# Optimization experiments

Hardware: AMD Instinct MI355X
Metric: run time of the kernel (lower is better)

Reference implementation:

```python
import jax, jax.numpy as jnp
import numpy as np

B, T, DIM, H, BUCKET = 4, 4096, 1024, 16, 64
E = DIM // H          # head dim = 64
U = T // BUCKET       # number of buckets = 64
EPS = 1e-6


def setup_inputs() -> dict:
    key = jax.random.key(0)
    ks = jax.random.split(key, 5)
    scale = 1.0 / np.sqrt(DIM)
    return {
        "x": jax.random.normal(ks[0], (B, T, DIM), dtype=jnp.float32),
        "Wq": jax.random.normal(ks[1], (DIM, DIM), dtype=jnp.float32) * scale,
        "Wk": jax.random.normal(ks[2], (DIM, DIM), dtype=jnp.float32) * scale,
        "Wv": jax.random.normal(ks[3], (DIM, DIM), dtype=jnp.float32) * scale,
        "Wo": jax.random.normal(ks[4], (DIM, DIM), dtype=jnp.float32) * scale,
        "bo": jnp.zeros((DIM,), dtype=jnp.float32),
    }


def _causal_linear_attn(q, k, v):
    # q, k, v: [b, h, t, e]; psi(k) = elu(k) + 1; q softmaxed over feature dim
    q = jax.nn.softmax(q, axis=-1)
    k = jax.nn.elu(k) + 1.0
    bucket = lambda x: x.reshape(*x.shape[:-2], U, BUCKET, E)  # [b,h,u,n,e]
    b_q, b_k, b_v = bucket(q), bucket(k), bucket(v)
    # cumulative key sums per bucket: [b,h,u,d]
    b_k_cumsum = jnp.cumsum(b_k.sum(axis=-2), axis=2)
    # per-bucket context then cumulative over buckets: [b,h,u,d,e]
    context = jnp.einsum("bhund,bhune->bhude", b_k, b_v)
    context = jnp.cumsum(context, axis=2)
    context = context / (b_k_cumsum[..., None] + EPS)
    # shift by one bucket (blindspot): bucket u sees context through bucket u-1
    context = jnp.concatenate(
        [jnp.zeros_like(context[:, :, :1]), context[:, :, :-1]], axis=2
    )
    attn = jnp.einsum("bhund,bhude->bhune", b_q, context)
    return attn.reshape(q.shape)  # [b,h,t,e]


def reference(x, Wq, Wk, Wv, Wo, bo):
    b, t, _ = x.shape
    q = x @ Wq
    k = x @ Wk
    v = x @ Wv
    merge = lambda z: z.reshape(b, t, H, E).transpose(0, 2, 1, 3)  # [b,h,t,e]
    attn = _causal_linear_attn(merge(q), merge(k), merge(v))
    out = attn.transpose(0, 2, 1, 3).reshape(b, t, DIM)
    return out @ Wo + bo
```

## Files before the change

kernel.cpp:

```cpp
#include <hip/hip_runtime.h>


#define T_LEN 4096
#define DIMN  1024
#define NHEAD 16
#define NB    4
#define MROWS (NB * T_LEN)

typedef float f32x4 __attribute__((ext_vector_type(4)));
typedef short s16x8 __attribute__((ext_vector_type(8)));
typedef short s16x4 __attribute__((ext_vector_type(4)));
using u16 = unsigned short;

__device__ __forceinline__ u16 f2bf(float f) {
  unsigned int u = __float_as_uint(f);
  u += 0x7fffu + ((u >> 16) & 1u);
  return (u16)(u >> 16);
}
__device__ __forceinline__ float bf2f(u16 h) {
  return __uint_as_float(((unsigned int)h) << 16);
}
__device__ __forceinline__ int swz16k(int off) {
  return off ^ (((off >> 7) & 3) << 4);
}

__global__ __launch_bounds__(256) void cvt_all_kern(const float* __restrict__ x,
                                                    const float* __restrict__ W0,
                                                    const float* __restrict__ W1,
                                                    const float* __restrict__ W2,
                                                    const float* __restrict__ W3,
                                                    u16* __restrict__ WT,
                                                    u16* __restrict__ xb) {
  __shared__ float tile[64][65];
  const int tid = threadIdx.x;
  if (blockIdx.x < 1024) {
    const int blk = blockIdx.x & 255;
    const int sel = blockIdx.x >> 8;
    const float* W = (sel == 0) ? W0 : (sel == 1) ? W1 : (sel == 2) ? W2 : W3;
    u16* dst = WT + (size_t)sel * DIMN * DIMN;
    const int k0 = (blk >> 4) << 6;
    const int n0 = (blk & 15) << 6;
    const int r = tid >> 6;
    const int c = tid & 63;
#pragma unroll
    for (int i = 0; i < 16; ++i) {
      int row = (i << 2) + r;
      tile[row][c] = W[(size_t)(k0 + row) * DIMN + n0 + c];
    }
    __syncthreads();
#pragma unroll
    for (int i = 0; i < 16; ++i) {
      int row = (i << 2) + r;
      dst[(size_t)(n0 + row) * DIMN + k0 + c] = f2bf(tile[c][row]);
    }
  } else {
    size_t i = ((size_t)(blockIdx.x - 1024) * 256 + tid) * 4;
    f32x4 v = *(const f32x4*)(x + i);
    s16x4 o;
    o.x = (short)f2bf(v.x); o.y = (short)f2bf(v.y);
    o.z = (short)f2bf(v.z); o.w = (short)f2bf(v.w);
    *(s16x4*)(xb + i) = o;
  }
}

template <int MODE>
__global__ __launch_bounds__(512, 4) void gemm_t(
    const u16* __restrict__ A, const u16* __restrict__ Bt,
    u16* __restrict__ dq, u16* __restrict__ dk, u16* __restrict__ dv,
    float* __restrict__ dO, const float* __restrict__ bias) {
  constexpr int K = 1024;
  constexpr int BNT = (MODE == 0) ? 12 : 4;
  constexpr int NT = K / 32;
  __shared__ char lds[73728];

  const int tid = threadIdx.x;
  const int l = tid & 63;
  const int w = tid >> 6;
  const int wm = w >> 2;
  const int wn = w & 3;

  const int xcd = (int)blockIdx.x & 7;
  const int idx = (int)blockIdx.x >> 3;
  const int g = idx / (4 * BNT);
  const int r2 = idx % (4 * BNT);
  const int bn = r2 >> 2;
  const int bm = xcd * 16 + g * 4 + (r2 & 3);
  const size_t arow0 = (size_t)bm * 128;
  const size_t brow0 = (size_t)bn * 256;

  int lrow[2], lcol[2];
#pragma unroll
  for (int i = 0; i < 2; ++i) {
    int lg = swz16k(tid * 16 + i * 8192);
    lrow[i] = lg >> 6;
    lcol[i] = (lg & 63) >> 1;
  }

  const int fr = l & 15;
  const int kswz = (((l >> 4) << 4)) ^ ((((fr >> 1) & 3)) << 4);

  auto STAGE = [&](int buf, int matsel, int tt) {
    const int kbase = (tt & (NT - 1)) * 32;
#pragma unroll
    for (int i = 0; i < 2; ++i) {
      if (matsel == 0 && i == 1) break;
      const u16* src = (matsel == 0)
          ? A  + (arow0 + (size_t)lrow[i]) * K + kbase + lcol[i]
          : Bt + (brow0 + (size_t)lrow[i]) * K + kbase + lcol[i];
      char* dst = lds + (buf * 24576 + matsel * 8192 + i * 8192 + tid * 16);
      __builtin_amdgcn_global_load_lds(
          (__attribute__((address_space(1))) const void*)src,
          (__attribute__((address_space(3))) void*)dst, 16, 0, 0);
    }
  };
  auto LDA = [&](int buf, int rowb) -> s16x8 {
    return *(const s16x8*)(lds + buf * 24576 + rowb * 64 + kswz);
  };
  auto LDB = [&](int buf, int rowb) -> s16x8 {
    return *(const s16x8*)(lds + buf * 24576 + 8192 + rowb * 64 + kswz);
  };

  f32x4 acc[4][4];
#pragma unroll
  for (int i = 0; i < 4; ++i)
#pragma unroll
    for (int j = 0; j < 4; ++j) acc[i][j] = {0.f, 0.f, 0.f, 0.f};

  STAGE(0, 0, 0); STAGE(0, 1, 0);
  STAGE(1, 0, 1); STAGE(1, 1, 1);
  asm volatile("s_waitcnt vmcnt(3)" ::: "memory");
  __builtin_amdgcn_sched_barrier(0);
  __builtin_amdgcn_s_barrier();

  const int amb = wm * 64;
  const int bnb = wn * 64;
  s16x8 af[4], bf[4];

  int bufR = 0, bufW = 2;
#pragma unroll 1
  for (int t = 0; t < NT; ++t) {
    STAGE(bufW, 0, t + 2);
    STAGE(bufW, 1, t + 2);
#pragma unroll
    for (int i = 0; i < 4; ++i) af[i] = LDA(bufR, amb + i * 16 + fr);
#pragma unroll
    for (int i = 0; i < 4; ++i) bf[i] = LDB(bufR, bnb + i * 16 + fr);
    __builtin_amdgcn_s_setprio(1);
#pragma unroll
    for (int mi = 0; mi < 4; ++mi)
#pragma unroll
      for (int ni = 0; ni < 4; ++ni)
        acc[mi][ni] = __builtin_amdgcn_mfma_f32_16x16x32_bf16(
            af[mi], bf[ni], acc[mi][ni], 0, 0, 0);
    __builtin_amdgcn_s_setprio(0);
    asm volatile("s_waitcnt vmcnt(3)" ::: "memory");
    __builtin_amdgcn_sched_barrier(0);
    __builtin_amdgcn_s_barrier();
    bufR = (bufR == 2) ? 0 : bufR + 1;
    bufW = (bufW == 2) ? 0 : bufW + 1;
  }

  const int r0 = (l >> 4) << 2;
  const int c0 = l & 15;
  if constexpr (MODE == 0) {
    const int mat = bn >> 2;
    u16* dst = (mat == 0) ? dq : ((mat == 1) ? dk : dv);
    const size_t colbase = (size_t)(bn & 3) * 256 + (size_t)wn * 64;
    if (mat == 0) {
#pragma unroll
      for (int mi = 0; mi < 4; ++mi) {
#pragma unroll
        for (int j = 0; j < 4; ++j) {
          float v0 = acc[mi][0][j], v1 = acc[mi][1][j];
          float v2 = acc[mi][2][j], v3 = acc[mi][3][j];
          float m = fmaxf(fmaxf(v0, v1), fmaxf(v2, v3));
#pragma unroll
          for (int off = 1; off < 16; off <<= 1) m = fmaxf(m, __shfl_xor(m, off));
          float e0 = __expf(v0 - m), e1 = __expf(v1 - m);
          float e2 = __expf(v2 - m), e3 = __expf(v3 - m);
          float s = e0 + e1 + e2 + e3;
#pragma unroll
          for (int off = 1; off < 16; off <<= 1) s += __shfl_xor(s, off);
          float inv = 1.f / s;
          const size_t row = arow0 + wm * 64 + mi * 16 + r0 + j;
          u16* p = dst + row * DIMN + colbase + c0;
          p[0]  = f2bf(e0 * inv); p[16] = f2bf(e1 * inv);
          p[32] = f2bf(e2 * inv); p[48] = f2bf(e3 * inv);
        }
      }
    } else {
#pragma unroll
      for (int mi = 0; mi < 4; ++mi)
#pragma unroll
        for (int ni = 0; ni < 4; ++ni)
#pragma unroll
          for (int j = 0; j < 4; ++j) {
            const size_t row = arow0 + wm * 64 + mi * 16 + r0 + j;
            float v = acc[mi][ni][j];
            float r = (mat == 1) ? (v > 0.f ? v + 1.f : __expf(v)) : v;
            dst[row * DIMN + colbase + ni * 16 + c0] = f2bf(r);
          }
    }
  } else {
#pragma unroll
    for (int mi = 0; mi < 4; ++mi)
#pragma unroll
      for (int ni = 0; ni < 4; ++ni) {
        const size_t col = brow0 + (size_t)wn * 64 + ni * 16 + c0;
        const float bv = bias[col];
#pragma unroll
        for (int j = 0; j < 4; ++j) {
          const size_t row = arow0 + wm * 64 + mi * 16 + r0 + j;
          dO[row * DIMN + col] = acc[mi][ni][j] + bv;
        }
      }
  }
}

__global__ __launch_bounds__(256) void ctx_bucket_kern(const u16* __restrict__ kb,
                                                       const u16* __restrict__ vb,
                                                       u16* __restrict__ ctx,
                                                       float* __restrict__ ksum) {
  __shared__ float kl[4096];
  __shared__ float vl[4096];
  const int blk = blockIdx.x;
  const int u = blk & 63;
  const int bh = blk >> 6;
  const int b = bh >> 4, h = bh & 15;
  const size_t rowbase = (size_t)b * T_LEN + (size_t)u * 64;
  const int tid = threadIdx.x;
#pragma unroll
  for (int i = 0; i < 16; ++i) {
    int idx = i * 256 + tid;
    int n = idx >> 6, d = idx & 63;
    size_t g = (rowbase + n) * DIMN + (size_t)h * 64 + d;
    kl[idx] = bf2f(kb[g]);
    vl[idx] = bf2f(vb[g]);
  }
  __syncthreads();
  const int dq = (tid & 15) << 2;
  const int eq = (tid >> 4) << 2;
  float a[4][4] = {};
  float ks[4] = {};
  for (int n = 0; n < 64; ++n) {
    f32x4 kv = *(const f32x4*)&kl[n * 64 + dq];
    f32x4 vv = *(const f32x4*)&vl[n * 64 + eq];
#pragma unroll
    for (int i = 0; i < 4; ++i) {
      ks[i] += kv[i];
#pragma unroll
      for (int j = 0; j < 4; ++j) a[i][j] += kv[i] * vv[j];
    }
  }
  const size_t cbase = (size_t)blk * 4096;
#pragma unroll
  for (int i = 0; i < 4; ++i) {
    s16x4 o;
    o.x = (short)f2bf(a[i][0]); o.y = (short)f2bf(a[i][1]);
    o.z = (short)f2bf(a[i][2]); o.w = (short)f2bf(a[i][3]);
    *(s16x4*)&ctx[cbase + (size_t)(dq + i) * 64 + eq] = o;
  }
  if ((tid >> 4) == 0) {
    f32x4 o = {ks[0], ks[1], ks[2], ks[3]};
    *(f32x4*)&ksum[(size_t)blk * 64 + dq] = o;
  }
}

__global__ __launch_bounds__(256) void ctx_cumnorm_kern(u16* __restrict__ ctx,
                                                        const float* __restrict__ ksum) {
  const int tid = blockIdx.x * 256 + threadIdx.x;
  const int bh = tid >> 10;
  const int rem = tid & 1023;
  const int d = rem >> 4;
  const int e0 = (rem & 15) << 2;
  float c0 = 0.f, c1 = 0.f, c2 = 0.f, c3 = 0.f, accK = 0.f;
  for (int u = 0; u < 64; ++u) {
    const size_t base = ((size_t)(bh * 64 + u)) * 4096 + (size_t)d * 64 + e0;
    s16x4 cv4 = *(const s16x4*)&ctx[base];
    float kk = ksum[(size_t)(bh * 64 + u) * 64 + d];
    float x0 = bf2f((u16)cv4.x), x1 = bf2f((u16)cv4.y);
    float x2 = bf2f((u16)cv4.z), x3 = bf2f((u16)cv4.w);
    s16x4 o;
    if (u == 0) {
      o.x = 0; o.y = 0; o.z = 0; o.w = 0;
    } else {
      float inv = 1.f / (accK + 1e-6f);
      o.x = (short)f2bf(c0 * inv); o.y = (short)f2bf(c1 * inv);
      o.z = (short)f2bf(c2 * inv); o.w = (short)f2bf(c3 * inv);
    }
    *(s16x4*)&ctx[base] = o;
    c0 += x0; c1 += x1; c2 += x2; c3 += x3;
    accK += kk;
  }
}

__global__ __launch_bounds__(256) void attn_bucket_kern(const u16* __restrict__ qb,
                                                        const u16* __restrict__ ctx,
                                                        u16* __restrict__ attn) {
  __shared__ float qT[64 * 68];
  __shared__ float cl[4096];
  const int blk = blockIdx.x;
  const int u = blk & 63;
  const int bh = blk >> 6;
  const int b = bh >> 4, h = bh & 15;
  const size_t rowbase = (size_t)b * T_LEN + (size_t)u * 64;
  const int tid = threadIdx.x;
  const size_t cbase = (size_t)blk * 4096;
#pragma unroll
  for (int i = 0; i < 16; ++i) {
    int idx = i * 256 + tid;
    int n = idx >> 6, d = idx & 63;
    qT[d * 68 + n] = bf2f(qb[(rowbase + n) * DIMN + (size_t)h * 64 + d]);
  }
#pragma unroll
  for (int i = 0; i < 4; ++i) {
    int idx4 = (i * 256 + tid) * 4;
    s16x4 cv = *(const s16x4*)&ctx[cbase + idx4];
    cl[idx4]     = bf2f((u16)cv.x);
    cl[idx4 + 1] = bf2f((u16)cv.y);
    cl[idx4 + 2] = bf2f((u16)cv.z);
    cl[idx4 + 3] = bf2f((u16)cv.w);
  }
  __syncthreads();
  const int nq = (tid & 15) << 2;
  const int eq = (tid >> 4) << 2;
  float a[4][4] = {};
  for (int d = 0; d < 64; ++d) {
    f32x4 qv = *(const f32x4*)&qT[d * 68 + nq];
    f32x4 cv = *(const f32x4*)&cl[d * 64 + eq];
#pragma unroll
    for (int i = 0; i < 4; ++i)
#pragma unroll
      for (int j = 0; j < 4; ++j) a[i][j] += qv[i] * cv[j];
  }
#pragma unroll
  for (int i = 0; i < 4; ++i) {
    s16x4 o;
    o.x = (short)f2bf(a[i][0]); o.y = (short)f2bf(a[i][1]);
    o.z = (short)f2bf(a[i][2]); o.w = (short)f2bf(a[i][3]);
    *(s16x4*)&attn[(rowbase + nq + i) * DIMN + (size_t)h * 64 + eq] = o;
  }
}

extern "C" void kernel_launch(void* const* d_in, const int* in_sizes, int n_in,
                              void* d_out, int out_size, void* d_ws, size_t ws_size,
                              hipStream_t stream) {
  const float* x  = (const float*)d_in[0];
  const float* Wq = (const float*)d_in[1];
  const float* Wk = (const float*)d_in[2];
  const float* Wv = (const float*)d_in[3];
  const float* Wo = (const float*)d_in[4];
  const float* bo = (const float*)d_in[5];
  float* out = (float*)d_out;

  constexpr size_t SZ_XB = (size_t)MROWS * DIMN * 2;
  constexpr size_t SZ_WT = (size_t)DIMN * DIMN * 2;
  constexpr size_t SZ_CTX = (size_t)NB * NHEAD * 64 * 64 * 64 * 2;
  char* ws = (char*)d_ws;
  u16*   xb   = (u16*)(ws);
  u16*   wqT  = (u16*)(ws + SZ_XB);
  u16*   woT  = (u16*)(ws + SZ_XB + 3 * SZ_WT);
  u16*   qb   = (u16*)(ws + SZ_XB + 4 * SZ_WT);
  u16*   kb   = (u16*)(ws + 2 * SZ_XB + 4 * SZ_WT);
  u16*   vb   = (u16*)(ws + 3 * SZ_XB + 4 * SZ_WT);
  u16*   ctx  = (u16*)(ws + 4 * SZ_XB + 4 * SZ_WT);
  float* ksum = (float*)(ws + 4 * SZ_XB + 4 * SZ_WT + SZ_CTX);
  u16*   attn = xb;

  cvt_all_kern<<<1024 + MROWS * DIMN / 1024, 256, 0, stream>>>(x, Wq, Wk, Wv, Wo,
                                                               wqT, xb);

  gemm_t<0><<<1536, 512, 0, stream>>>(xb, wqT, qb, kb, vb, nullptr, nullptr);

  ctx_bucket_kern<<<NB * NHEAD * 64, 256, 0, stream>>>(kb, vb, ctx, ksum);
  ctx_cumnorm_kern<<<256, 256, 0, stream>>>(ctx, ksum);
  attn_bucket_kern<<<NB * NHEAD * 64, 256, 0, stream>>>(qb, ctx, attn);

  gemm_t<1><<<512, 512, 0, stream>>>(attn, woT, nullptr, nullptr, nullptr, out, bo);
}
```

Measured before the change: 268.2 us.

## Use MFMA for bucket context and attention with transposed K/V layout

The QKV GEMM epilogue now writes K and V transposed as [b,h,d,t], so each wave can load MFMA fragments directly from global memory without an LDS transpose. The per-bucket K^T V context and the Q·context products are rewritten as one-wave-per-bucket bf16 MFMA kernels in place of the scalar FP32 LDS loops. The stored context is transposed to match, and the cumulative-normalise kernel is adjusted to the new layout. This removes LDS staging and scalar FMA work. In exchange the transposed epilogue stores and the scattered bf16 stores in the new kernels are less coalesced.

Measured after the change: 247.0 us. 7.9% less time.

```diff
diff --git a/kernel.cpp b/kernel.cpp
--- a/kernel.cpp
+++ b/kernel.cpp
@@ -164,9 +164,9 @@
   const int c0 = l & 15;
   if constexpr (MODE == 0) {
     const int mat = bn >> 2;
-    u16* dst = (mat == 0) ? dq : ((mat == 1) ? dk : dv);
-    const size_t colbase = (size_t)(bn & 3) * 256 + (size_t)wn * 64;
     if (mat == 0) {
+      u16* dst = dq;
+      const size_t colbase = (size_t)(bn & 3) * 256 + (size_t)wn * 64;
 #pragma unroll
       for (int mi = 0; mi < 4; ++mi) {
 #pragma unroll
@@ -189,17 +189,27 @@
         }
       }
     } else {
-#pragma unroll
-      for (int mi = 0; mi < 4; ++mi)
-#pragma unroll
-        for (int ni = 0; ni < 4; ++ni)
+      u16* dst = (mat == 1) ? dk : dv;
+      const int colb = (bn & 3) * 256 + wn * 64;
+#pragma unroll
+      for (int mi = 0; mi < 4; ++mi) {
+        const size_t row = arow0 + wm * 64 + mi * 16 + r0;
+        const int bb = (int)(row >> 12);
+        const int t = (int)(row & 4095);
+#pragma unroll
+        for (int ni = 0; ni < 4; ++ni) {
+          const int col = colb + ni * 16 + c0;
+          const int h = col >> 6, d = col & 63;
+          s16x4 o;
 #pragma unroll
           for (int j = 0; j < 4; ++j) {
-            const size_t row = arow0 + wm * 64 + mi * 16 + r0 + j;
             float v = acc[mi][ni][j];
             float r = (mat == 1) ? (v > 0.f ? v + 1.f : __expf(v)) : v;
-            dst[row * DIMN + colbase + ni * 16 + c0] = f2bf(r);
+            o[j] = (short)f2bf(r);
           }
+          *(s16x4*)&dst[((size_t)((bb * 16 + h) * 64 + d)) * 4096 + t] = o;
+        }
+      }
     }
   } else {
 #pragma unroll
@@ -217,129 +227,152 @@
   }
 }
 
-__global__ __launch_bounds__(256) void ctx_bucket_kern(const u16* __restrict__ kb,
-                                                       const u16* __restrict__ vb,
-                                                       u16* __restrict__ ctx,
-                                                       float* __restrict__ ksum) {
-  __shared__ float kl[4096];
-  __shared__ float vl[4096];
-  const int blk = blockIdx.x;
-  const int u = blk & 63;
-  const int bh = blk >> 6;
-  const int b = bh >> 4, h = bh & 15;
-  const size_t rowbase = (size_t)b * T_LEN + (size_t)u * 64;
+__global__ __launch_bounds__(256) void ctx_mfma_kern(const u16* __restrict__ kT,
+                                                     const u16* __restrict__ vT,
+                                                     u16* __restrict__ ctxT,
+                                                     float* __restrict__ ksum) {
   const int tid = threadIdx.x;
-#pragma unroll
-  for (int i = 0; i < 16; ++i) {
-    int idx = i * 256 + tid;
-    int n = idx >> 6, d = idx & 63;
-    size_t g = (rowbase + n) * DIMN + (size_t)h * 64 + d;
-    kl[idx] = bf2f(kb[g]);
-    vl[idx] = bf2f(vb[g]);
-  }
-  __syncthreads();
-  const int dq = (tid & 15) << 2;
-  const int eq = (tid >> 4) << 2;
-  float a[4][4] = {};
-  float ks[4] = {};
-  for (int n = 0; n < 64; ++n) {
-    f32x4 kv = *(const f32x4*)&kl[n * 64 + dq];
-    f32x4 vv = *(const f32x4*)&vl[n * 64 + eq];
-#pragma unroll
-    for (int i = 0; i < 4; ++i) {
-      ks[i] += kv[i];
-#pragma unroll
-      for (int j = 0; j < 4; ++j) a[i][j] += kv[i] * vv[j];
-    }
-  }
-  const size_t cbase = (size_t)blk * 4096;
-#pragma unroll
-  for (int i = 0; i < 4; ++i) {
-    s16x4 o;
-    o.x = (short)f2bf(a[i][0]); o.y = (short)f2bf(a[i][1]);
-    o.z = (short)f2bf(a[i][2]); o.w = (short)f2bf(a[i][3]);
-    *(s16x4*)&ctx[cbase + (size_t)(dq + i) * 64 + eq] = o;
-  }
-  if ((tid >> 4) == 0) {
-    f32x4 o = {ks[0], ks[1], ks[2], ks[3]};
-    *(f32x4*)&ksum[(size_t)blk * 64 + dq] = o;
-  }
-}
-
-__global__ __launch_bounds__(256) void ctx_cumnorm_kern(u16* __restrict__ ctx,
+  const int l = tid & 63;
+  const int w = tid >> 6;
+  const int bh = (int)blockIdx.x >> 4;
+  const int u = (((int)blockIdx.x & 15) << 2) + w;
+  const size_t tbase = (size_t)bh * 64 * 4096 + (size_t)u * 64;
+  const int fr = l & 15;
+  const int kg = (l >> 4) << 3;
+
+  s16x8 a[4][2], b[4][2];
+#pragma unroll
+  for (int mi = 0; mi < 4; ++mi)
+#pragma unroll
+    for (int kk = 0; kk < 2; ++kk)
+      a[mi][kk] = *(const s16x8*)&vT[tbase + (size_t)(mi * 16 + fr) * 4096 +
+                                     kk * 32 + kg];
+#pragma unroll
+  for (int ni = 0; ni < 4; ++ni)
+#pragma unroll
+    for (int kk = 0; kk < 2; ++kk)
+      b[ni][kk] = *(const s16x8*)&kT[tbase + (size_t)(ni * 16 + fr) * 4096 +
+                                     kk * 32 + kg];
+
+  f32x4 acc[4][4];
+#pragma unroll
+  for (int i = 0; i < 4; ++i)
+#pragma unroll
+    for (int j = 0; j < 4; ++j) acc[i][j] = {0.f, 0.f, 0.f, 0.f};
+#pragma unroll
+  for (int mi = 0; mi < 4; ++mi)
+#pragma unroll
+    for (int ni = 0; ni < 4; ++ni)
+#pragma unroll
+      for (int kk = 0; kk < 2; ++kk)
+        acc[mi][ni] = __builtin_amdgcn_mfma_f32_16x16x32_bf16(
+            a[mi][kk], b[ni][kk], acc[mi][ni], 0, 0, 0);
+
+  const size_t kbase = ((size_t)bh * 64 + u) * 64;
+#pragma unroll
+  for (int ni = 0; ni < 4; ++ni) {
+    float s = 0.f;
+#pragma unroll
+    for (int kk = 0; kk < 2; ++kk)
+#pragma unroll
+      for (int j = 0; j < 8; ++j) s += bf2f((u16)b[ni][kk][j]);
+    s += __shfl_xor(s, 16);
+    s += __shfl_xor(s, 32);
+    if (l < 16) ksum[kbase + ni * 16 + l] = s;
+  }
+
+  const size_t cbase = kbase * 64;
+  const int r0 = (l >> 4) << 2;
+#pragma unroll
+  for (int mi = 0; mi < 4; ++mi)
+#pragma unroll
+    for (int ni = 0; ni < 4; ++ni)
+#pragma unroll
+      for (int j = 0; j < 4; ++j)
+        ctxT[cbase + (size_t)(mi * 16 + r0 + j) * 64 + ni * 16 + fr] =
+            f2bf(acc[mi][ni][j]);
+}
+
+__global__ __launch_bounds__(256) void ctx_cumnorm_kern(u16* __restrict__ ctxT,
                                                         const float* __restrict__ ksum) {
   const int tid = blockIdx.x * 256 + threadIdx.x;
   const int bh = tid >> 10;
   const int rem = tid & 1023;
-  const int d = rem >> 4;
-  const int e0 = (rem & 15) << 2;
-  float c0 = 0.f, c1 = 0.f, c2 = 0.f, c3 = 0.f, accK = 0.f;
+  const int e = rem >> 4;
+  const int d0 = (rem & 15) << 2;
+  f32x4 c = {0.f, 0.f, 0.f, 0.f};
+  f32x4 accK = {0.f, 0.f, 0.f, 0.f};
   for (int u = 0; u < 64; ++u) {
-    const size_t base = ((size_t)(bh * 64 + u)) * 4096 + (size_t)d * 64 + e0;
-    s16x4 cv4 = *(const s16x4*)&ctx[base];
-    float kk = ksum[(size_t)(bh * 64 + u) * 64 + d];
-    float x0 = bf2f((u16)cv4.x), x1 = bf2f((u16)cv4.y);
-    float x2 = bf2f((u16)cv4.z), x3 = bf2f((u16)cv4.w);
+    const size_t cb = (((size_t)(bh * 64 + u)) * 64 + e) * 64 + d0;
+    s16x4 raw = *(const s16x4*)&ctxT[cb];
+    f32x4 kk = *(const f32x4*)&ksum[((size_t)(bh * 64 + u)) * 64 + d0];
     s16x4 o;
     if (u == 0) {
       o.x = 0; o.y = 0; o.z = 0; o.w = 0;
     } else {
-      float inv = 1.f / (accK + 1e-6f);
-      o.x = (short)f2bf(c0 * inv); o.y = (short)f2bf(c1 * inv);
-      o.z = (short)f2bf(c2 * inv); o.w = (short)f2bf(c3 * inv);
+      o.x = (short)f2bf(c.x / (accK.x + 1e-6f));
+      o.y = (short)f2bf(c.y / (accK.y + 1e-6f));
+      o.z = (short)f2bf(c.z / (accK.z + 1e-6f));
+      o.w = (short)f2bf(c.w / (accK.w + 1e-6f));
     }
-    *(s16x4*)&ctx[base] = o;
-    c0 += x0; c1 += x1; c2 += x2; c3 += x3;
+    *(s16x4*)&ctxT[cb] = o;
+    c.x += bf2f((u16)raw.x); c.y += bf2f((u16)raw.y);
+    c.z += bf2f((u16)raw.z); c.w += bf2f((u16)raw.w);
     accK += kk;
   }
 }
 
-__global__ __launch_bounds__(256) void attn_bucket_kern(const u16* __restrict__ qb,
-                                                        const u16* __restrict__ ctx,
-                                                        u16* __restrict__ attn) {
-  __shared__ float qT[64 * 68];
-  __shared__ float cl[4096];
-  const int blk = blockIdx.x;
-  const int u = blk & 63;
-  const int bh = blk >> 6;
+__global__ __launch_bounds__(256) void attn_mfma_kern(const u16* __restrict__ qb,
+                                                      const u16* __restrict__ ctxT,
+                                                      u16* __restrict__ attn) {
+  const int tid = threadIdx.x;
+  const int l = tid & 63;
+  const int w = tid >> 6;
+  const int bh = (int)blockIdx.x >> 4;
+  const int u = (((int)blockIdx.x & 15) << 2) + w;
   const int b = bh >> 4, h = bh & 15;
   const size_t rowbase = (size_t)b * T_LEN + (size_t)u * 64;
-  const int tid = threadIdx.x;
-  const size_t cbase = (size_t)blk * 4096;
-#pragma unroll
-  for (int i = 0; i < 16; ++i) {
-    int idx = i * 256 + tid;
-    int n = idx >> 6, d = idx & 63;
-    qT[d * 68 + n] = bf2f(qb[(rowbase + n) * DIMN + (size_t)h * 64 + d]);
-  }
-#pragma unroll
-  for (int i = 0; i < 4; ++i) {
-    int idx4 = (i * 256 + tid) * 4;
-    s16x4 cv = *(const s16x4*)&ctx[cbase + idx4];
-    cl[idx4]     = bf2f((u16)cv.x);
-    cl[idx4 + 1] = bf2f((u16)cv.y);
-    cl[idx4 + 2] = bf2f((u16)cv.z);
-    cl[idx4 + 3] = bf2f((u16)cv.w);
-  }
-  __syncthreads();
-  const int nq = (tid & 15) << 2;
-  const int eq = (tid >> 4) << 2;
-  float a[4][4] = {};
-  for (int d = 0; d < 64; ++d) {
-    f32x4 qv = *(const f32x4*)&qT[d * 68 + nq];
-    f32x4 cv = *(const f32x4*)&cl[d * 64 + eq];
-#pragma unroll
-    for (int i = 0; i < 4; ++i)
-#pragma unroll
-      for (int j = 0; j < 4; ++j) a[i][j] += qv[i] * cv[j];
-  }
-#pragma unroll
-  for (int i = 0; i < 4; ++i) {
-    s16x4 o;
-    o.x = (short)f2bf(a[i][0]); o.y = (short)f2bf(a[i][1]);
-    o.z = (short)f2bf(a[i][2]); o.w = (short)f2bf(a[i][3]);
-    *(s16x4*)&attn[(rowbase + nq + i) * DIMN + (size_t)h * 64 + eq] = o;
-  }
+  const size_t cbase = ((size_t)bh * 64 + u) * 4096;
+  const int fr = l & 15;
+  const int kg = (l >> 4) << 3;
+
+  s16x8 a[4][2], bfr[4][2];
+#pragma unroll
+  for (int mi = 0; mi < 4; ++mi)
+#pragma unroll
+    for (int kk = 0; kk < 2; ++kk)
+      a[mi][kk] = *(const s16x8*)&qb[(rowbase + mi * 16 + fr) * DIMN +
+                                     (size_t)h * 64 + kk * 32 + kg];
+#pragma unroll
+  for (int ni = 0; ni < 4; ++ni)
+#pragma unroll
+    for (int kk = 0; kk < 2; ++kk)
+      bfr[ni][kk] = *(const s16x8*)&ctxT[cbase + (size_t)(ni * 16 + fr) * 64 +
+                                         kk * 32 + kg];
+
+  f32x4 acc[4][4];
+#pragma unroll
+  for (int i = 0; i < 4; ++i)
+#pragma unroll
+    for (int j = 0; j < 4; ++j) acc[i][j] = {0.f, 0.f, 0.f, 0.f};
+#pragma unroll
+  for (int mi = 0; mi < 4; ++mi)
+#pragma unroll
+    for (int ni = 0; ni < 4; ++ni)
+#pragma unroll
+      for (int kk = 0; kk < 2; ++kk)
+        acc[mi][ni] = __builtin_amdgcn_mfma_f32_16x16x32_bf16(
+            a[mi][kk], bfr[ni][kk], acc[mi][ni], 0, 0, 0);
+
+  const int r0 = (l >> 4) << 2;
+#pragma unroll
+  for (int mi = 0; mi < 4; ++mi)
+#pragma unroll
+    for (int ni = 0; ni < 4; ++ni)
+#pragma unroll
+      for (int j = 0; j < 4; ++j)
+        attn[(rowbase + mi * 16 + r0 + j) * DIMN + (size_t)h * 64 +
+             ni * 16 + fr] = f2bf(acc[mi][ni][j]);
 }
 
 extern "C" void kernel_launch(void* const* d_in, const int* in_sizes, int n_in,
@@ -361,20 +394,20 @@
   u16*   wqT  = (u16*)(ws + SZ_XB);
   u16*   woT  = (u16*)(ws + SZ_XB + 3 * SZ_WT);
   u16*   qb   = (u16*)(ws + SZ_XB + 4 * SZ_WT);
-  u16*   kb   = (u16*)(ws + 2 * SZ_XB + 4 * SZ_WT);
-  u16*   vb   = (u16*)(ws + 3 * SZ_XB + 4 * SZ_WT);
-  u16*   ctx  = (u16*)(ws + 4 * SZ_XB + 4 * SZ_WT);
+  u16*   kT   = (u16*)(ws + 2 * SZ_XB + 4 * SZ_WT);
+  u16*   vT   = (u16*)(ws + 3 * SZ_XB + 4 * SZ_WT);
+  u16*   ctxT = (u16*)(ws + 4 * SZ_XB + 4 * SZ_WT);
   float* ksum = (float*)(ws + 4 * SZ_XB + 4 * SZ_WT + SZ_CTX);
   u16*   attn = xb;
 
   cvt_all_kern<<<1024 + MROWS * DIMN / 1024, 256, 0, stream>>>(x, Wq, Wk, Wv, Wo,
                                                                wqT, xb);
 
-  gemm_t<0><<<1536, 512, 0, stream>>>(xb, wqT, qb, kb, vb, nullptr, nullptr);
-
-  ctx_bucket_kern<<<NB * NHEAD * 64, 256, 0, stream>>>(kb, vb, ctx, ksum);
-  ctx_cumnorm_kern<<<256, 256, 0, stream>>>(ctx, ksum);
-  attn_bucket_kern<<<NB * NHEAD * 64, 256, 0, stream>>>(qb, ctx, attn);
+  gemm_t<0><<<1536, 512, 0, stream>>>(xb, wqT, qb, kT, vT, nullptr, nullptr);
+
+  ctx_mfma_kern<<<NB * NHEAD * 16, 256, 0, stream>>>(kT, vT, ctxT, ksum);
+  ctx_cumnorm_kern<<<256, 256, 0, stream>>>(ctxT, ksum);
+  attn_mfma_kern<<<NB * NHEAD * 16, 256, 0, stream>>>(qb, ctxT, attn);
 
   gemm_t<1><<<512, 512, 0, stream>>>(attn, woT, nullptr, nullptr, nullptr, out, bo);
 }
```
